# Performance work log

Hardware: AMD Instinct MI355X
Metric: run time of the kernel (lower is better)

The kernel has to match this reference:

```python
import jax, jax.numpy as jnp
import numpy as np

D = 128; DFF = 256; NH = 4; HD = D // NH
B = 8; T = 1024
PAIRS = [(0, 1), (1, 2), (0, 2)]  # (ABSTRACT,DYNAMIC),(DYNAMIC,CONCRETE),(ABSTRACT,CONCRETE)
BW = 0.5 / 3.0   # bridge_weight / len(BRIDGE_PAIRS)
LB_W = 0.01


def _hex_np():
    # itertools.product([-1,1], repeat=6): index i = 6-bit binary of i, MSB first, 0->-1
    bits = (np.arange(64)[:, None] >> np.arange(5, -1, -1)) & 1
    return (bits * 2.0 - 1.0).astype(np.float32)


def _anchors_np():
    h = _hex_np()
    idx = {'GEO': 0, 'HYDRO': 18, 'PYRO': 45, 'AERO': 6, 'COSMO': 27, 'NOOS': 63}
    a = (h[idx['NOOS']] + h[idx['COSMO']]) / 2.0   # ABSTRACT
    d = (h[idx['AERO']] + h[idx['PYRO']]) / 2.0    # DYNAMIC
    c = (h[idx['GEO']] + h[idx['HYDRO']]) / 2.0    # CONCRETE
    return np.stack([a, d, c]).astype(np.float32)


def _ln(x, g, b, eps=1e-5):
    m = x.mean(-1, keepdims=True)
    v = ((x - m) ** 2).mean(-1, keepdims=True)
    return (x - m) * jax.lax.rsqrt(v + eps) * g + b


def _mha(q, kv, in_w, out_w):
    # torch nn.MultiheadAttention, bias=False, batch_first
    Bq, Tq, _ = q.shape
    wq, wk, wv = in_w[:D], in_w[D:2 * D], in_w[2 * D:]
    Q = (q @ wq.T).reshape(Bq, Tq, NH, HD)
    K = (kv @ wk.T).reshape(Bq, Tq, NH, HD)
    V = (kv @ wv.T).reshape(Bq, Tq, NH, HD)
    scores = jnp.einsum('bqhd,bkhd->bhqk', Q, K) / jnp.sqrt(jnp.float32(HD))
    attn = jax.nn.softmax(scores, axis=-1)
    o = jnp.einsum('bhqk,bkhd->bqhd', attn, V).reshape(Bq, Tq, D)
    return o @ out_w.T


def setup_inputs() -> dict:
    key = jax.random.key(0)
    ks = iter(jax.random.split(key, 40))
    r = lambda shape, s=0.02: jax.random.normal(next(ks), shape, dtype=jnp.float32) * s
    return {
        'x': jax.random.normal(next(ks), (B, T, D), dtype=jnp.float32),
        'gr_norm_g': jnp.ones((D,), jnp.float32), 'gr_norm_b': jnp.zeros((D,), jnp.float32),
        'q6_w': r((6, D), 0.1),
        'log_temp': jnp.log(jnp.float32(0.5)),
        'grp_norm_g': jnp.ones((3, D), jnp.float32), 'grp_norm_b': jnp.zeros((3, D), jnp.float32),
        'grp_proj_w': r((3, 2, D), 0.1), 'grp_proj_b': jnp.zeros((3, 2), jnp.float32),
        'me_norm_g': jnp.ones((6, D), jnp.float32), 'me_norm_b': jnp.zeros((6, D), jnp.float32),
        'me_gate_w': r((6, DFF, D)), 'me_val_w': r((6, DFF, D)), 'me_out_w': r((6, D, DFF)),
        'br_in_w': r((3, 3 * D, D)), 'br_out_w': r((3, D, D)),
        'br_nq_g': jnp.ones((3, D), jnp.float32), 'br_nq_b': jnp.zeros((3, D), jnp.float32),
        'br_nkv_g': jnp.ones((3, D), jnp.float32), 'br_nkv_b': jnp.zeros((3, D), jnp.float32),
        'br_nffn_g': jnp.ones((3, D), jnp.float32), 'br_nffn_b': jnp.zeros((3, D), jnp.float32),
        'br_gate_w': r((3, 2 * D, D)), 'br_val_w': r((3, 2 * D, D)), 'br_ffn_out_w': r((3, D, 2 * D)),
        'br_gate': jnp.full((3,), -2.0, dtype=jnp.float32),
        'out_norm_g': jnp.ones((D,), jnp.float32), 'out_norm_b': jnp.zeros((D,), jnp.float32),
        'out_w': r((D, D)),
    }


def reference(x, gr_norm_g, gr_norm_b, q6_w, log_temp, grp_norm_g, grp_norm_b,
              grp_proj_w, grp_proj_b, me_norm_g, me_norm_b, me_gate_w, me_val_w,
              me_out_w, br_in_w, br_out_w, br_nq_g, br_nq_b, br_nkv_g, br_nkv_b,
              br_nffn_g, br_nffn_b, br_gate_w, br_val_w, br_ffn_out_w, br_gate,
              out_norm_g, out_norm_b, out_w):
    hexg = jnp.asarray(_hex_np())        # (64, 6)
    anchors = jnp.asarray(_anchors_np())  # (3, 6)

    # ---- GlobalRouter ----
    h = _ln(x, gr_norm_g, gr_norm_b)
    soft_bits = jnp.tanh(h @ q6_w.T)                       # (B,T,6)
    sim = soft_bits @ hexg.T                               # (B,T,64)
    temp = jnp.clip(jnp.exp(log_temp), 0.1, 5.0)
    hex_w = jax.nn.softmax(sim / temp, axis=-1)
    soft_hex = hex_w @ hexg                                # (B,T,6)
    group_weights = jax.nn.softmax(soft_hex @ anchors.T, axis=-1)  # (B,T,3)
    mw = group_weights.mean(axis=(0, 1))
    lb_total = -(mw * jnp.log(mw + 1e-8)).sum()

    # ---- all 6 micro experts (per-expert LayerNorm shares x's stats) ----
    m = x.mean(-1, keepdims=True)
    v = ((x - m) ** 2).mean(-1, keepdims=True)
    xn = (x - m) * jax.lax.rsqrt(v + 1e-5)                 # (B,T,D)
    hme = xn[None] * me_norm_g[:, None, None, :] + me_norm_b[:, None, None, :]  # (6,B,T,D)
    gate = jax.nn.silu(jnp.einsum('ebtd,efd->ebtf', hme, me_gate_w))
    val = jnp.einsum('ebtd,efd->ebtf', hme, me_val_w)
    eo = jnp.einsum('ebtf,edf->ebtd', gate * val, me_out_w)  # (6,B,T,D)

    # ---- per-group routing (2 experts each, top_k=2) ----
    group_outs = []
    for g in range(3):  # groups ordered [ABSTRACT, DYNAMIC, CONCRETE]; experts [2g, 2g+1]
        hg = xn * grp_norm_g[g] + grp_norm_b[g]
        logits = hg @ grp_proj_w[g].T + grp_proj_b[g]      # (B,T,2)
        w = jax.nn.softmax(logits, axis=-1)
        vals, idx = jax.lax.top_k(w, 2)                    # k = min(top_k=2, n=2)
        sparse = (jax.nn.one_hot(idx, 2, dtype=w.dtype) * vals[..., None]).sum(-2)
        sparse = sparse / (sparse.sum(-1, keepdims=True) + 1e-8)
        mwg = w.mean(axis=(0, 1))
        lb_total = lb_total - (mwg * jnp.log(mwg + 1e-8)).sum()
        go = sparse[..., 0:1] * eo[2 * g] + sparse[..., 1:2] * eo[2 * g + 1]
        group_outs.append(group_weights[..., g:g + 1] * go)

    # ---- bridge experts ----
    bridge_sum = jnp.zeros_like(x)
    for i, (a, b) in enumerate(PAIRS):
        xq, xk = group_outs[a], group_outs[b]
        qn = _ln(xq, br_nq_g[i], br_nq_b[i])
        kvn = _ln(xk, br_nkv_g[i], br_nkv_b[i])
        xb = xq + _mha(qn, kvn, br_in_w[i], br_out_w[i])
        hb = _ln(xb, br_nffn_g[i], br_nffn_b[i])
        ff = (jax.nn.silu(hb @ br_gate_w[i].T) * (hb @ br_val_w[i].T)) @ br_ffn_out_w[i].T
        xb = (xb + ff) * jax.nn.sigmoid(br_gate[i])
        bridge_sum = bridge_sum + BW * xb

    combined = group_outs[0] + group_outs[1] + group_outs[2] + bridge_sum
    out = _ln(combined, out_norm_g, out_norm_b) @ out_w.T
    return out, lb_total * LB_W
```

## Files before the change

kernel.cpp:

```cpp
#include <hip/hip_runtime.h>
#include <math.h>

#define DD    128
#define DFF   256
#define NHH   4
#define HDD   32
#define BB    8
#define TT    1024
#define NTOK  (BB*TT)
#define LDK   72
#define QKVN  384

#define WB_MEGATE 0
#define WB_MEVAL  196608
#define WB_MEOUT  393216
#define WB_BRIN   589824
#define WB_BROUT  737280
#define WB_BRG    786432
#define WB_BRV    884736
#define WB_BRF    983040
#define WB_OUTW   1081344
#define WB_TOT    1097728

typedef __bf16 bf16x8 __attribute__((ext_vector_type(8)));
typedef float  f32x4  __attribute__((ext_vector_type(4)));

__device__ __forceinline__ float wsum(float v){
#pragma unroll
  for(int o=32;o>0;o>>=1) v += __shfl_xor(v,o,64);
  return v;
}
__device__ __forceinline__ float wmaxr(float v){
#pragma unroll
  for(int o=32;o>0;o>>=1) v = fmaxf(v,__shfl_xor(v,o,64));
  return v;
}
__device__ __forceinline__ unsigned short f2bf(float x){
  __bf16 h = (__bf16)x;
  unsigned short u;
  __builtin_memcpy(&u, &h, 2);
  return u;
}

__device__ __forceinline__ void stage16(const float* __restrict__ gp,
                                        unsigned short* __restrict__ dst){
  float4 f0 = *reinterpret_cast<const float4*>(gp);
  float4 f1 = *reinterpret_cast<const float4*>(gp+4);
  float4 f2 = *reinterpret_cast<const float4*>(gp+8);
  float4 f3 = *reinterpret_cast<const float4*>(gp+12);
  float f[16] = {f0.x,f0.y,f0.z,f0.w, f1.x,f1.y,f1.z,f1.w,
                 f2.x,f2.y,f2.z,f2.w, f3.x,f3.y,f3.z,f3.w};
  unsigned short h[16];
#pragma unroll
  for(int j=0;j<16;j++) h[j] = f2bf(f[j]);
  *reinterpret_cast<uint4*>(dst)   = *reinterpret_cast<const uint4*>(h);
  *reinterpret_cast<uint4*>(dst+8) = *reinterpret_cast<const uint4*>(h+8);
}

__device__ __forceinline__ void stage16bf(const unsigned short* __restrict__ gp,
                                          unsigned short* __restrict__ dst){
  const uint4* s = reinterpret_cast<const uint4*>(gp);
  *reinterpret_cast<uint4*>(dst)   = s[0];
  *reinterpret_cast<uint4*>(dst+8) = s[1];
}

__device__ __forceinline__ void stageLN(const float* __restrict__ fr,
                                        float mean, float rstd,
                                        const float* __restrict__ g,
                                        const float* __restrict__ b,
                                        unsigned short* __restrict__ dst){
  unsigned short h[16];
#pragma unroll
  for(int j=0;j<16;j++){
    float y = (fr[j]-mean)*rstd*g[j] + b[j];
    h[j] = f2bf(y);
  }
  *reinterpret_cast<uint4*>(dst)   = *reinterpret_cast<const uint4*>(h);
  *reinterpret_cast<uint4*>(dst+8) = *reinterpret_cast<const uint4*>(h+8);
}

__global__ __launch_bounds__(256) void wconv(
    const float* __restrict__ a0, const float* __restrict__ a1, const float* __restrict__ a2,
    const float* __restrict__ a3, const float* __restrict__ a4, const float* __restrict__ a5,
    const float* __restrict__ a6, const float* __restrict__ a7, const float* __restrict__ a8,
    unsigned short* __restrict__ dst, float qsc){
  size_t i = ((size_t)blockIdx.x*256 + threadIdx.x)*4;
  if(i >= WB_TOT) return;
  const float* s; size_t off = i; float sc = 1.0f;
  if(i < WB_MEVAL){ s=a0; }
  else if(i < WB_MEOUT){ s=a1; off = i-WB_MEVAL; }
  else if(i < WB_BRIN ){ s=a2; off = i-WB_MEOUT; }
  else if(i < WB_BROUT){ s=a3; off = i-WB_BRIN;
    int row = (int)(off>>7); if((row % 384) < 128) sc = qsc; }
  else if(i < WB_BRG ){ s=a4; off = i-WB_BROUT; }
  else if(i < WB_BRV ){ s=a5; off = i-WB_BRG; }
  else if(i < WB_BRF ){ s=a6; off = i-WB_BRV; }
  else if(i < WB_OUTW){ s=a7; off = i-WB_BRF; }
  else { s=a8; off = i-WB_OUTW; }
  float4 v = *reinterpret_cast<const float4*>(s + off);
  unsigned short h4[4] = {f2bf(v.x*sc), f2bf(v.y*sc), f2bf(v.z*sc), f2bf(v.w*sc)};
  *reinterpret_cast<uint2*>(dst + i) = *reinterpret_cast<const uint2*>(h4);
}

__global__ __launch_bounds__(256) void routing_kernel(
    const float* __restrict__ x,
    const float* __restrict__ gr_g, const float* __restrict__ gr_b,
    const float* __restrict__ q6,   const float* __restrict__ logtemp,
    const float* __restrict__ grp_g,const float* __restrict__ grp_b,
    const float* __restrict__ gpw,  const float* __restrict__ gpb,
    float* __restrict__ gw_out, float* __restrict__ coef, float* __restrict__ part){
  __shared__ float sp[4][9];
  int lane = threadIdx.x & 63;
  int wv   = threadIdx.x >> 6;
  int t    = (blockIdx.x<<2) + wv;
  const float* xr = x + (size_t)t*DD;
  float r0 = xr[lane], r1 = xr[lane+64];
  float mn = wsum(r0+r1) * (1.0f/DD);
  float d0 = r0-mn, d1 = r1-mn;
  float vv = wsum(d0*d0 + d1*d1) * (1.0f/DD);
  float rstd = rsqrtf(vv + 1e-5f);
  float x0 = d0*rstd, x1 = d1*rstd;
  float h0 = x0*gr_g[lane]+gr_b[lane];
  float h1 = x1*gr_g[lane+64]+gr_b[lane+64];
  float sb[6];
#pragma unroll
  for(int j=0;j<6;j++){
    float p = h0*q6[j*DD+lane] + h1*q6[j*DD+lane+64];
    sb[j] = tanhf(wsum(p));
  }
  float sim = 0.f;
#pragma unroll
  for(int j=0;j<6;j++) sim += ((lane>>(5-j))&1) ? sb[j] : -sb[j];
  float temp = expf(logtemp[0]); temp = fminf(fmaxf(temp,0.1f),5.0f);
  float mx = wmaxr(sim);
  float p  = expf((sim-mx)/temp);
  float w  = p / wsum(p);
  float sh[6];
#pragma unroll
  for(int j=0;j<6;j++) sh[j] = wsum(((lane>>(5-j))&1) ? w : -w);
  const float A0[6]={0,1,1,0,1,1}, A1[6]={0,-1,0,1,0,0}, A2[6]={-1,0,-1,-1,0,-1};
  float l0=0,l1=0,l2=0;
#pragma unroll
  for(int j=0;j<6;j++){ l0+=sh[j]*A0[j]; l1+=sh[j]*A1[j]; l2+=sh[j]*A2[j]; }
  float m3 = fmaxf(l0,fmaxf(l1,l2));
  float e0=expf(l0-m3), e1=expf(l1-m3), e2=expf(l2-m3);
  float inv3 = 1.0f/(e0+e1+e2);
  float g0=e0*inv3, g1=e1*inv3, g2=e2*inv3;
  if(lane==0){ gw_out[t*3]=g0; gw_out[t*3+1]=g1; gw_out[t*3+2]=g2; }
  float gwv[3]={g0,g1,g2};
  float pw[6];
#pragma unroll
  for(int g=0; g<3; g++){
    float hg0 = x0*grp_g[g*DD+lane]    + grp_b[g*DD+lane];
    float hg1 = x1*grp_g[g*DD+lane+64] + grp_b[g*DD+lane+64];
    float q0 = wsum(hg0*gpw[(g*2+0)*DD+lane] + hg1*gpw[(g*2+0)*DD+lane+64]) + gpb[g*2+0];
    float q1 = wsum(hg0*gpw[(g*2+1)*DD+lane] + hg1*gpw[(g*2+1)*DD+lane+64]) + gpb[g*2+1];
    float mm = fmaxf(q0,q1);
    float a0 = expf(q0-mm), a1 = expf(q1-mm);
    float inv = 1.0f/(a0+a1);
    float w0 = a0*inv, w1 = a1*inv;
    pw[g*2]=w0; pw[g*2+1]=w1;
    float invs = 1.0f/(w0+w1+1e-8f);
    if(lane==0){
      coef[(size_t)(2*g  )*NTOK + t] = gwv[g]*w0*invs;
      coef[(size_t)(2*g+1)*NTOK + t] = gwv[g]*w1*invs;
    }
  }
  if(lane==0){
    sp[wv][0]=g0; sp[wv][1]=g1; sp[wv][2]=g2;
#pragma unroll
    for(int k=0;k<6;k++) sp[wv][3+k]=pw[k];
  }
  __syncthreads();
  if(threadIdx.x<9){
    part[blockIdx.x*9+threadIdx.x] =
      sp[0][threadIdx.x]+sp[1][threadIdx.x]+sp[2][threadIdx.x]+sp[3][threadIdx.x];
  }
}

__global__ __launch_bounds__(256) void lb_kernel(const float* __restrict__ part, float* __restrict__ outlb){
  __shared__ float sm[4][9];
  float acc[9] = {};
  for(int i=threadIdx.x; i<2048; i+=256){
#pragma unroll
    for(int c=0;c<9;c++) acc[c] += part[i*9+c];
  }
#pragma unroll
  for(int c=0;c<9;c++) acc[c] = wsum(acc[c]);
  int wv = threadIdx.x>>6, lane = threadIdx.x&63;
  if(lane==0){
#pragma unroll
    for(int c=0;c<9;c++) sm[wv][c]=acc[c];
  }
  __syncthreads();
  if(threadIdx.x==0){
    const float invN = 1.0f/(float)NTOK;
    float lb=0;
#pragma unroll
    for(int c=0;c<9;c++){
      float s = sm[0][c]+sm[1][c]+sm[2][c]+sm[3][c];
      float mw = s*invN;
      lb -= mw*logf(mw+1e-8f);
    }
    outlb[0] = lb*0.01f;
  }
}

template<int MODE,int LN,int ABF,int OBF,int PSEL,int RSEL,int SUM,int QKV>
__global__ __launch_bounds__(256) void gemm_mfma(
    const void* __restrict__ Ap, const unsigned short* __restrict__ W, void* __restrict__ Cp,
    int M, int N, int K,
    const float* __restrict__ sv, const float* __restrict__ bv,
    const float* __restrict__ resid, const float* __restrict__ gptr,
    size_t az, size_t wz, size_t cz, size_t pz, size_t rz, size_t gz){
  __shared__ unsigned short As[64*LDK];
  __shared__ unsigned short Ws[64*LDK];
  const int z = blockIdx.z;
  const float* A = (const float*)Ap;
  const unsigned short* Ab = (const unsigned short*)Ap;
  if(QKV){
    bool isQ = (blockIdx.x < 2);
    int s = isQ ? ((z==1)?1:0) : ((z==0)?1:2);
    A += (size_t)s*NTOK*DD;
    if(!isQ){ sv = resid; bv = gptr; }
  } else if(PSEL==0){ A += z*az; Ab += z*az; }
  else if(PSEL==1){ int s = (z==1)?1:0; A += (size_t)s*NTOK*DD; Ab += (size_t)s*NTOK*DD; }
  else            { int s = (z==0)?1:2; A += (size_t)s*NTOK*DD; Ab += (size_t)s*NTOK*DD; }
  W += z*wz;
  float* C = (float*)Cp + z*cz;
  unsigned short* Cb = (unsigned short*)Cp + z*cz;
  const float* rs = resid;
  if(RSEL==0) rs += z*rz;
  else { int s = (z==1)?1:0; rs += (size_t)s*NTOK*DD; }
  sv += z*pz; bv += z*pz;
  const float* gp2 = gptr + z*gz;
  int tid  = threadIdx.x;
  int m0   = blockIdx.y*64, n0 = blockIdx.x*64;
  int w    = tid>>6, lane = tid&63;
  int wr   = (w>>1)*32, wc = (w&1)*32;
  int r    = tid>>2, seg = (tid&3)*16;
  f32x4 acc[2][2] = {};
  auto step = [&](){
#pragma unroll
    for(int kk=0;kk<64;kk+=32){
      int ko = kk + (lane>>4)*8;
      bf16x8 a0 = *reinterpret_cast<const bf16x8*>(&As[(wr    + (lane&15))*LDK + ko]);
      bf16x8 a1 = *reinterpret_cast<const bf16x8*>(&As[(wr+16 + (lane&15))*LDK + ko]);
      bf16x8 b0 = *reinterpret_cast<const bf16x8*>(&Ws[(wc    + (lane&15))*LDK + ko]);
      bf16x8 b1 = *reinterpret_cast<const bf16x8*>(&Ws[(wc+16 + (lane&15))*LDK + ko]);
      acc[0][0] = __builtin_amdgcn_mfma_f32_16x16x32_bf16(a0,b0,acc[0][0],0,0,0);
      acc[0][1] = __builtin_amdgcn_mfma_f32_16x16x32_bf16(a0,b1,acc[0][1],0,0,0);
      acc[1][0] = __builtin_amdgcn_mfma_f32_16x16x32_bf16(a1,b0,acc[1][0],0,0,0);
      acc[1][1] = __builtin_amdgcn_mfma_f32_16x16x32_bf16(a1,b1,acc[1][1],0,0,0);
    }
  };
  if(LN){
    float fr[32]; float mean, rstd;
    if(SUM){
#pragma unroll
      for(int j=0;j<32;j++) fr[j]=0.f;
#pragma unroll
      for(int s=0;s<3;s++){
        const float* r1 = A     + (size_t)s*NTOK*DD + (size_t)(m0+r)*K + seg;
        const float* r2 = resid + (size_t)s*NTOK*DD + (size_t)(m0+r)*K + seg;
#pragma unroll
        for(int j=0;j<4;j++){
          float4 v1 = *reinterpret_cast<const float4*>(r1 + j*4);
          float4 v2 = *reinterpret_cast<const float4*>(r2 + j*4);
          fr[j*4]+=v1.x+v2.x; fr[j*4+1]+=v1.y+v2.y; fr[j*4+2]+=v1.z+v2.z; fr[j*4+3]+=v1.w+v2.w;
          float4 w1 = *reinterpret_cast<const float4*>(r1 + 64 + j*4);
          float4 w2 = *reinterpret_cast<const float4*>(r2 + 64 + j*4);
          fr[16+j*4]+=w1.x+w2.x; fr[16+j*4+1]+=w1.y+w2.y; fr[16+j*4+2]+=w1.z+w2.z; fr[16+j*4+3]+=w1.w+w2.w;
        }
      }
    } else {
      const float* arow = A + (size_t)(m0+r)*K + seg;
#pragma unroll
      for(int j=0;j<4;j++) *reinterpret_cast<float4*>(&fr[j*4])    = *reinterpret_cast<const float4*>(arow + j*4);
#pragma unroll
      for(int j=0;j<4;j++) *reinterpret_cast<float4*>(&fr[16+j*4]) = *reinterpret_cast<const float4*>(arow + 64 + j*4);
    }
    float s1=0.f, s2=0.f;
#pragma unroll
    for(int j=0;j<32;j++){ s1 += fr[j]; s2 += fr[j]*fr[j]; }
    s1 += __shfl_xor(s1,1,64); s1 += __shfl_xor(s1,2,64);
    s2 += __shfl_xor(s2,1,64); s2 += __shfl_xor(s2,2,64);
    mean = s1*(1.0f/DD);
    float var = s2*(1.0f/DD) - mean*mean;
    rstd = rsqrtf(var + 1e-5f);
#pragma unroll
    for(int kh=0; kh<2; ++kh){
      __syncthreads();
      stageLN(fr + kh*16, mean, rstd, sv + kh*64 + seg, bv + kh*64 + seg, &As[r*LDK + seg]);
      stage16bf(W + (size_t)(n0+r)*K + kh*64 + seg, &Ws[r*LDK + seg]);
      __syncthreads();
      step();
    }
  } else {
    for(int k0=0;k0<K;k0+=64){
      __syncthreads();
      if(ABF) stage16bf(Ab + (size_t)(m0+r)*K + k0 + seg, &As[r*LDK + seg]);
      else    stage16(A  + (size_t)(m0+r)*K + k0 + seg, &As[r*LDK + seg]);
      stage16bf(W + (size_t)(n0+r)*K + k0 + seg, &Ws[r*LDK + seg]);
      __syncthreads();
      step();
    }
  }
#pragma unroll
  for(int i=0;i<2;i++){
#pragma unroll
    for(int j=0;j<2;j++){
      int mb = m0 + wr + i*16 + (lane>>4)*4;
      int n  = n0 + wc + j*16 + (lane&15);
#pragma unroll
      for(int rg=0;rg<4;rg++){
        int m = mb + rg;
        float v = acc[i][j][rg];
        size_t o = (size_t)m*N + n;
        if(MODE==0){ if(OBF) Cb[o] = f2bf(v); else C[o] = v; }
        else if(MODE==3){ C[o] = rs[o] + v; }
        else if(MODE==5){
          float gs = (0.5f/3.0f)/(1.0f+expf(-gp2[0]));
          C[o] = gs*(rs[o]+v);
        }
      }
    }
  }
}

__global__ __launch_bounds__(256) void gemm_dual(
    const float* __restrict__ A, const unsigned short* __restrict__ G,
    const unsigned short* __restrict__ V,
    unsigned short* __restrict__ C, int M, int N, int K,
    const float* __restrict__ sv, const float* __restrict__ bv,
    size_t az, size_t wz, size_t cz, size_t pz){
  __shared__ unsigned short As[64*LDK];
  __shared__ unsigned short Gs[64*LDK];
  __shared__ unsigned short Vs[64*LDK];
  const int z = blockIdx.z;
  A += z*az; G += z*wz; V += z*wz; C += z*cz; sv += z*pz; bv += z*pz;
  int tid  = threadIdx.x;
  int m0   = blockIdx.y*64, n0 = blockIdx.x*64;
  int w    = tid>>6, lane = tid&63;
  int wr   = (w>>1)*32, wc = (w&1)*32;
  int r    = tid>>2, seg = (tid&3)*16;
  f32x4 accg[2][2] = {};
  f32x4 accv[2][2] = {};
  float fr[32]; float mean, rstd;
  {
    const float* arow = A + (size_t)(m0+r)*K + seg;
#pragma unroll
    for(int j=0;j<4;j++) *reinterpret_cast<float4*>(&fr[j*4])    = *reinterpret_cast<const float4*>(arow + j*4);
#pragma unroll
    for(int j=0;j<4;j++) *reinterpret_cast<float4*>(&fr[16+j*4]) = *reinterpret_cast<const float4*>(arow + 64 + j*4);
    float s1=0.f, s2=0.f;
#pragma unroll
    for(int j=0;j<32;j++){ s1 += fr[j]; s2 += fr[j]*fr[j]; }
    s1 += __shfl_xor(s1,1,64); s1 += __shfl_xor(s1,2,64);
    s2 += __shfl_xor(s2,1,64); s2 += __shfl_xor(s2,2,64);
    mean = s1*(1.0f/DD);
    float var = s2*(1.0f/DD) - mean*mean;
    rstd = rsqrtf(var + 1e-5f);
  }
#pragma unroll
  for(int kh=0; kh<2; ++kh){
    int k0 = kh*64;
    __syncthreads();
    stageLN(fr + kh*16, mean, rstd, sv + k0 + seg, bv + k0 + seg, &As[r*LDK + seg]);
    stage16bf(G + (size_t)(n0+r)*K + k0 + seg, &Gs[r*LDK + seg]);
    stage16bf(V + (size_t)(n0+r)*K + k0 + seg, &Vs[r*LDK + seg]);
    __syncthreads();
#pragma unroll
    for(int kk=0;kk<64;kk+=32){
      int ko = kk + (lane>>4)*8;
      bf16x8 a0 = *reinterpret_cast<const bf16x8*>(&As[(wr    + (lane&15))*LDK + ko]);
      bf16x8 a1 = *reinterpret_cast<const bf16x8*>(&As[(wr+16 + (lane&15))*LDK + ko]);
      bf16x8 g0 = *reinterpret_cast<const bf16x8*>(&Gs[(wc    + (lane&15))*LDK + ko]);
      bf16x8 g1 = *reinterpret_cast<const bf16x8*>(&Gs[(wc+16 + (lane&15))*LDK + ko]);
      bf16x8 v0 = *reinterpret_cast<const bf16x8*>(&Vs[(wc    + (lane&15))*LDK + ko]);
      bf16x8 v1 = *reinterpret_cast<const bf16x8*>(&Vs[(wc+16 + (lane&15))*LDK + ko]);
      accg[0][0] = __builtin_amdgcn_mfma_f32_16x16x32_bf16(a0,g0,accg[0][0],0,0,0);
      accg[0][1] = __builtin_amdgcn_mfma_f32_16x16x32_bf16(a0,g1,accg[0][1],0,0,0);
      accg[1][0] = __builtin_amdgcn_mfma_f32_16x16x32_bf16(a1,g0,accg[1][0],0,0,0);
      accg[1][1] = __builtin_amdgcn_mfma_f32_16x16x32_bf16(a1,g1,accg[1][1],0,0,0);
      accv[0][0] = __builtin_amdgcn_mfma_f32_16x16x32_bf16(a0,v0,accv[0][0],0,0,0);
      accv[0][1] = __builtin_amdgcn_mfma_f32_16x16x32_bf16(a0,v1,accv[0][1],0,0,0);
      accv[1][0] = __builtin_amdgcn_mfma_f32_16x16x32_bf16(a1,v0,accv[1][0],0,0,0);
      accv[1][1] = __builtin_amdgcn_mfma_f32_16x16x32_bf16(a1,v1,accv[1][1],0,0,0);
    }
  }
#pragma unroll
  for(int i=0;i<2;i++){
#pragma unroll
    for(int j=0;j<2;j++){
      int mb = m0 + wr + i*16 + (lane>>4)*4;
      int n  = n0 + wc + j*16 + (lane&15);
#pragma unroll
      for(int rg=0;rg<4;rg++){
        float gg = accg[i][j][rg];
        float vv = accv[i][j][rg];
        float sg = gg/(1.0f+expf(-gg));
        C[(size_t)(mb+rg)*N + n] = f2bf(sg*vv);
      }
    }
  }
}

__global__ __launch_bounds__(256) void gemm_moe2(
    const unsigned short* __restrict__ Ab, const unsigned short* __restrict__ Wb,
    float* __restrict__ Cb, const float* __restrict__ coef){
  __shared__ unsigned short As0[64*LDK];
  __shared__ unsigned short As1[64*LDK];
  __shared__ unsigned short Ws0[64*LDK];
  __shared__ unsigned short Ws1[64*LDK];
  const int g = blockIdx.z;
  const unsigned short* A0 = Ab + (size_t)(2*g)*NTOK*DFF;
  const unsigned short* A1 = A0 + (size_t)NTOK*DFF;
  const unsigned short* W0 = Wb + (size_t)(2*g)*DD*DFF;
  const unsigned short* W1 = W0 + (size_t)DD*DFF;
  float* C = Cb + (size_t)g*NTOK*DD;
  const float* c0 = coef + (size_t)(2*g)*NTOK;
  const float* c1 = c0 + NTOK;
  int tid  = threadIdx.x;
  int m0   = blockIdx.y*64, n0 = blockIdx.x*64;
  int w    = tid>>6, lane = tid&63;
  int wr   = (w>>1)*32, wc = (w&1)*32;
  int r    = tid>>2, seg = (tid&3)*16;
  f32x4 a0acc[2][2] = {};
  f32x4 a1acc[2][2] = {};
  for(int k0=0;k0<DFF;k0+=64){
    __syncthreads();
    stage16bf(A0 + (size_t)(m0+r)*DFF + k0 + seg, &As0[r*LDK + seg]);
    stage16bf(A1 + (size_t)(m0+r)*DFF + k0 + seg, &As1[r*LDK + seg]);
    stage16bf(W0 + (size_t)(n0+r)*DFF + k0 + seg, &Ws0[r*LDK + seg]);
    stage16bf(W1 + (size_t)(n0+r)*DFF + k0 + seg, &Ws1[r*LDK + seg]);
    __syncthreads();
#pragma unroll
    for(int kk=0;kk<64;kk+=32){
      int ko = kk + (lane>>4)*8;
      bf16x8 x00 = *reinterpret_cast<const bf16x8*>(&As0[(wr    + (lane&15))*LDK + ko]);
      bf16x8 x01 = *reinterpret_cast<const bf16x8*>(&As0[(wr+16 + (lane&15))*LDK + ko]);
      bf16x8 x10 = *reinterpret_cast<const bf16x8*>(&As1[(wr    + (lane&15))*LDK + ko]);
      bf16x8 x11 = *reinterpret_cast<const bf16x8*>(&As1[(wr+16 + (lane&15))*LDK + ko]);
      bf16x8 w00 = *reinterpret_cast<const bf16x8*>(&Ws0[(wc    + (lane&15))*LDK + ko]);
      bf16x8 w01 = *reinterpret_cast<const bf16x8*>(&Ws0[(wc+16 + (lane&15))*LDK + ko]);
      bf16x8 w10 = *reinterpret_cast<const bf16x8*>(&Ws1[(wc    + (lane&15))*LDK + ko]);
      bf16x8 w11 = *reinterpret_cast<const bf16x8*>(&Ws1[(wc+16 + (lane&15))*LDK + ko]);
      a0acc[0][0] = __builtin_amdgcn_mfma_f32_16x16x32_bf16(x00,w00,a0acc[0][0],0,0,0);
      a0acc[0][1] = __builtin_amdgcn_mfma_f32_16x16x32_bf16(x00,w01,a0acc[0][1],0,0,0);
      a0acc[1][0] = __builtin_amdgcn_mfma_f32_16x16x32_bf16(x01,w00,a0acc[1][0],0,0,0);
      a0acc[1][1] = __builtin_amdgcn_mfma_f32_16x16x32_bf16(x01,w01,a0acc[1][1],0,0,0);
      a1acc[0][0] = __builtin_amdgcn_mfma_f32_16x16x32_bf16(x10,w10,a1acc[0][0],0,0,0);
      a1acc[0][1] = __builtin_amdgcn_mfma_f32_16x16x32_bf16(x10,w11,a1acc[0][1],0,0,0);
      a1acc[1][0] = __builtin_amdgcn_mfma_f32_16x16x32_bf16(x11,w10,a1acc[1][0],0,0,0);
      a1acc[1][1] = __builtin_amdgcn_mfma_f32_16x16x32_bf16(x11,w11,a1acc[1][1],0,0,0);
    }
  }
#pragma unroll
  for(int i=0;i<2;i++){
#pragma unroll
    for(int j=0;j<2;j++){
      int mb = m0 + wr + i*16 + (lane>>4)*4;
      int n  = n0 + wc + j*16 + (lane&15);
#pragma unroll
      for(int rg=0;rg<4;rg++){
        int m = mb + rg;
        C[(size_t)m*DD + n] = c0[m]*a0acc[i][j][rg] + c1[m]*a1acc[i][j][rg];
      }
    }
  }
}

#define PSW(row) (((row)&8)<<1)
#define VSW(row) ((((row)>>3)&3)<<3)
__global__ __launch_bounds__(256) void attn_fused(
    const unsigned short* __restrict__ qkv,
    unsigned short* __restrict__ obuf){
  __shared__ __align__(16) unsigned short Ks[2][64*40];
  __shared__ __align__(16) unsigned short Vt[2][32*72];
  __shared__ __align__(16) unsigned short Vones[16*72];
  __shared__ __align__(16) unsigned short Ps[4][16*72];
  const int tid = threadIdx.x;
  const int w = tid>>6, lane = tid&63;
  const int lr = lane&15, lg = lane>>4;
  const int n_  = blockIdx.x;
  const int kx  = n_ & 7, jx = n_ >> 3;
  const int grp = kx*12 + (jx>>4);
  const int bx  = jx & 15;
  const int h   = grp & 3;
  const int b   = (grp>>2) & 7;
  const int br  = grp >> 5;
  const int qtok0 = b*TT + bx*64 + w*16;
  for(int idx=tid; idx<16*72; idx+=256)
    Vones[idx] = (idx < 64) ? (unsigned short)0x3F80 : (unsigned short)0;
  const unsigned short* qp = qkv + (size_t)br*NTOK*QKVN + (size_t)(qtok0 + lr)*QKVN + h*HDD + lg*8;
  bf16x8 qa = *reinterpret_cast<const bf16x8*>(qp);
  f32x4 o0 = {}, o1 = {}, o2 = {};
  float m[4] = {-1e30f,-1e30f,-1e30f,-1e30f};
  const unsigned short* KVbase = qkv + (size_t)br*NTOK*QKVN + (size_t)(b*TT)*QKVN + DD + h*HDD;
  const int skey0 = (tid    )>>3, sseg0 = ((tid    )&7)*4;
  const int skey1 = (tid+256)>>3, sseg1 = ((tid+256)&7)*4;

  {
    const unsigned short* s0 = KVbase + (size_t)skey0*QKVN + sseg0;
    const unsigned short* s1 = KVbase + (size_t)skey1*QKVN + sseg1;
    uint2 k0v = *reinterpret_cast<const uint2*>(s0);
    uint2 v0v = *reinterpret_cast<const uint2*>(s0 + DD);
    uint2 k1v = *reinterpret_cast<const uint2*>(s1);
    uint2 v1v = *reinterpret_cast<const uint2*>(s1 + DD);
    *reinterpret_cast<uint2*>(&Ks[0][skey0*40+sseg0]) = k0v;
    *reinterpret_cast<uint2*>(&Ks[0][skey1*40+sseg1]) = k1v;
    unsigned short vs[4];
    *reinterpret_cast<uint2*>(vs) = v0v;
    { const int kc = skey0 ^ VSW(sseg0);
      Vt[0][(sseg0  )*72+kc]=vs[0]; Vt[0][(sseg0+1)*72+kc]=vs[1];
      Vt[0][(sseg0+2)*72+kc]=vs[2]; Vt[0][(sseg0+3)*72+kc]=vs[3]; }
    *reinterpret_cast<uint2*>(vs) = v1v;
    { const int kc = skey1 ^ VSW(sseg1);
      Vt[0][(sseg1  )*72+kc]=vs[0]; Vt[0][(sseg1+1)*72+kc]=vs[1];
      Vt[0][(sseg1+2)*72+kc]=vs[2]; Vt[0][(sseg1+3)*72+kc]=vs[3]; }
  }
  __syncthreads();

  for(int t=0; t<16; t++){
    const int cur = t & 1;
    uint2 kn0, vn0, kn1, vn1;
    if(t < 15){
      const unsigned short* s0 = KVbase + (size_t)((t+1)*64 + skey0)*QKVN + sseg0;
      const unsigned short* s1 = KVbase + (size_t)((t+1)*64 + skey1)*QKVN + sseg1;
      kn0 = *reinterpret_cast<const uint2*>(s0);
      vn0 = *reinterpret_cast<const uint2*>(s0 + DD);
      kn1 = *reinterpret_cast<const uint2*>(s1);
      vn1 = *reinterpret_cast<const uint2*>(s1 + DD);
    }
    f32x4 s[4];
#pragma unroll
    for(int f=0;f<4;f++){
      bf16x8 kb = *reinterpret_cast<const bf16x8*>(&Ks[cur][(f*16+lr)*40 + lg*8]);
      f32x4 z = {};
      s[f] = __builtin_amdgcn_mfma_f32_16x16x32_bf16(qa,kb,z,0,0,0);
    }
    float tmax[4]; bool need=false;
#pragma unroll
    for(int r=0;r<4;r++){
      tmax[r] = fmaxf(fmaxf(s[0][r],s[1][r]),fmaxf(s[2][r],s[3][r]));
      need = need || (tmax[r] > m[r] + 8.0f);
    }
    if(__any(need)){
#pragma unroll
      for(int r=0;r<4;r++){
        float t2 = tmax[r];
#pragma unroll
        for(int off=1;off<16;off<<=1) t2 = fmaxf(t2,__shfl_xor(t2,off,64));
        float nm = fmaxf(m[r],t2);
        float sc = __builtin_amdgcn_exp2f(m[r]-nm);
        m[r] = nm; o0[r] *= sc; o1[r] *= sc; o2[r] *= sc;
      }
    }
#pragma unroll
    for(int r=0;r<4;r++){
      const int q = lg*4+r;
      const int cw = PSW(q);
#pragma unroll
      for(int f=0;f<4;f++){
        float p = __builtin_amdgcn_exp2f(s[f][r]-m[r]);
        Ps[w][q*72 + ((f*16+lr)^cw)] = f2bf(p);
      }
    }
    const int pw_ = PSW(lr);
    bf16x8 pa0 = *reinterpret_cast<const bf16x8*>(&Ps[w][lr*72 + ((lg*8   )^pw_)]);
    bf16x8 pa1 = *reinterpret_cast<const bf16x8*>(&Ps[w][lr*72 + ((lg*8+32)^pw_)]);
    {
      const int r_ = lr, vw = VSW(r_);
      bf16x8 vb0 = *reinterpret_cast<const bf16x8*>(&Vt[cur][r_*72 + ((lg*8   )^vw)]);
      bf16x8 vb1 = *reinterpret_cast<const bf16x8*>(&Vt[cur][r_*72 + ((lg*8+32)^vw)]);
      o0 = __builtin_amdgcn_mfma_f32_16x16x32_bf16(pa0,vb0,o0,0,0,0);
      o0 = __builtin_amdgcn_mfma_f32_16x16x32_bf16(pa1,vb1,o0,0,0,0);
    }
    {
      const int r_ = 16+lr, vw = VSW(r_);
      bf16x8 vb0 = *reinterpret_cast<const bf16x8*>(&Vt[cur][(r_-16)*72 + ((lg*8   )^vw)+16*72]);
      bf16x8 vb1 = *reinterpret_cast<const bf16x8*>(&Vt[cur][(r_-16)*72 + ((lg*8+32)^vw)+16*72]);
      o1 = __builtin_amdgcn_mfma_f32_16x16x32_bf16(pa0,vb0,o1,0,0,0);
      o1 = __builtin_amdgcn_mfma_f32_16x16x32_bf16(pa1,vb1,o1,0,0,0);
    }
    {
      const int r_ = 32+lr, vw = VSW(r_);
      bf16x8 vb0 = *reinterpret_cast<const bf16x8*>(&Vones[lr*72 + ((lg*8   )^vw)]);
      bf16x8 vb1 = *reinterpret_cast<const bf16x8*>(&Vones[lr*72 + ((lg*8+32)^vw)]);
      o2 = __builtin_amdgcn_mfma_f32_16x16x32_bf16(pa0,vb0,o2,0,0,0);
      o2 = __builtin_amdgcn_mfma_f32_16x16x32_bf16(pa1,vb1,o2,0,0,0);
    }
    if(t < 15){
      const int nb = cur ^ 1;
      *reinterpret_cast<uint2*>(&Ks[nb][skey0*40+sseg0]) = kn0;
      *reinterpret_cast<uint2*>(&Ks[nb][skey1*40+sseg1]) = kn1;
      unsigned short vs[4];
      *reinterpret_cast<uint2*>(vs) = vn0;
      { const int kc = skey0 ^ VSW(sseg0);
        Vt[nb][(sseg0  )*72+kc]=vs[0]; Vt[nb][(sseg0+1)*72+kc]=vs[1];
        Vt[nb][(sseg0+2)*72+kc]=vs[2]; Vt[nb][(sseg0+3)*72+kc]=vs[3]; }
      *reinterpret_cast<uint2*>(vs) = vn1;
      { const int kc = skey1 ^ VSW(sseg1);
        Vt[nb][(sseg1  )*72+kc]=vs[0]; Vt[nb][(sseg1+1)*72+kc]=vs[1];
        Vt[nb][(sseg1+2)*72+kc]=vs[2]; Vt[nb][(sseg1+3)*72+kc]=vs[3]; }
    }
    __syncthreads();
  }
#pragma unroll
  for(int r=0;r<4;r++){
    float lsr = __shfl(o2[r], lane & 48, 64);
    float inv = 1.0f/lsr;
    int row = qtok0 + lg*4 + r;
    unsigned short* orow = obuf + (size_t)br*NTOK*DD + (size_t)row*DD + h*HDD;
    orow[lr]    = f2bf(o0[r]*inv);
    orow[16+lr] = f2bf(o1[r]*inv);
  }
}

extern "C" void kernel_launch(void* const* d_in, const int* in_sizes, int n_in,
                              void* d_out, int out_size, void* d_ws, size_t ws_size,
                              hipStream_t stream){
  (void)in_sizes; (void)n_in; (void)out_size; (void)ws_size;
  const float* x       = (const float*)d_in[0];
  const float* gr_g    = (const float*)d_in[1];
  const float* gr_b    = (const float*)d_in[2];
  const float* q6_w    = (const float*)d_in[3];
  const float* logtemp = (const float*)d_in[4];
  const float* grp_g   = (const float*)d_in[5];
  const float* grp_b   = (const float*)d_in[6];
  const float* gpw     = (const float*)d_in[7];
  const float* gpb     = (const float*)d_in[8];
  const float* me_g    = (const float*)d_in[9];
  const float* me_b    = (const float*)d_in[10];
  const float* me_gate = (const float*)d_in[11];
  const float* me_val  = (const float*)d_in[12];
  const float* me_out  = (const float*)d_in[13];
  const float* br_in   = (const float*)d_in[14];
  const float* br_outw = (const float*)d_in[15];
  const float* nq_g    = (const float*)d_in[16];
  const float* nq_b    = (const float*)d_in[17];
  const float* nkv_g   = (const float*)d_in[18];
  const float* nkv_b   = (const float*)d_in[19];
  const float* nff_g   = (const float*)d_in[20];
  const float* nff_b   = (const float*)d_in[21];
  const float* brg_w   = (const float*)d_in[22];
  const float* brv_w   = (const float*)d_in[23];
  const float* brf_w   = (const float*)d_in[24];
  const float* br_gate = (const float*)d_in[25];
  const float* on_g    = (const float*)d_in[26];
  const float* on_b    = (const float*)d_in[27];
  const float* out_w   = (const float*)d_in[28];
  float* out = (float*)d_out;
  float* ws  = (float*)d_ws;

  float* coef  = ws;
  float* part  = ws + 65536;
  unsigned short* gvb6 = (unsigned short*)(ws + 131072);
  float* go    = ws + 6731072;
  unsigned short* qkv  = (unsigned short*)(ws + 9900000);
  unsigned short* obuf = (unsigned short*)(ws + 14700000);
  unsigned short* wbf  = (unsigned short*)(ws + 21400000);
  float* xb    = ws + 23000000;
  unsigned short* gvb2 = (unsigned short*)(ws + 26200000);
  float* bsum  = ws + 29400000;
  float* gw    = ws + 32700000;

  const float qscale = 0.17677669529663687f * 1.4426950408889634f;

  wconv<<<1072,256,0,stream>>>(me_gate, me_val, me_out, br_in, br_outw,
                               brg_w, brv_w, brf_w, out_w, wbf, qscale);

  routing_kernel<<<2048,256,0,stream>>>(x, gr_g, gr_b, q6_w, logtemp,
                                        grp_g, grp_b, gpw, gpb, gw, coef, part);
  lb_kernel<<<1,256,0,stream>>>(part, out + 1048576);

  gemm_dual<<<dim3(4,128,6),256,0,stream>>>(x, wbf+WB_MEGATE, wbf+WB_MEVAL, gvb6,
      NTOK,DFF,DD, me_g, me_b, 0, (size_t)DFF*DD, (size_t)NTOK*DFF, DD);
  gemm_moe2<<<dim3(2,128,3),256,0,stream>>>(gvb6, wbf+WB_MEOUT, go, coef);

  gemm_mfma<0,1,0,1,0,0,0,1><<<dim3(6,128,3),256,0,stream>>>(go, wbf+WB_BRIN, qkv,
      NTOK,QKVN,DD, nq_g, nq_b, nkv_g, nkv_b,
      0, (size_t)QKVN*DD, (size_t)NTOK*QKVN, DD, 0, 0);
  attn_fused<<<1536,256,0,stream>>>(qkv, obuf);
  gemm_mfma<3,0,1,0,0,1,0,0><<<dim3(2,128,3),256,0,stream>>>(obuf, wbf+WB_BROUT, xb,
      NTOK,DD,DD, nullptr, nullptr, go, nullptr,
      (size_t)NTOK*DD, (size_t)DD*DD, (size_t)NTOK*DD, 0, 0, 0);
  gemm_dual<<<dim3(4,128,3),256,0,stream>>>(xb, wbf+WB_BRG, wbf+WB_BRV, gvb2,
      NTOK,2*DD,DD, nff_g, nff_b, (size_t)NTOK*DD, (size_t)2*DD*DD, (size_t)NTOK*2*DD, DD);
  gemm_mfma<5,0,1,0,0,0,0,0><<<dim3(2,128,3),256,0,stream>>>(gvb2, wbf+WB_BRF, bsum,
      NTOK,DD,2*DD, nullptr, nullptr, xb, br_gate,
      (size_t)NTOK*2*DD, (size_t)DD*2*DD, (size_t)NTOK*DD, 0, (size_t)NTOK*DD, 1);

  gemm_mfma<0,1,0,0,0,0,1,0><<<dim3(2,128,1),256,0,stream>>>(go, wbf+WB_OUTW, out,
      NTOK,DD,DD, on_g, on_b, bsum, nullptr,
      0, 0, 0, 0, 0, 0);
}
```

Before: 191.1 us.

## Process 128 queries per attention block with 8 waves sharing K/V tiles

The attention kernel now runs 512 threads (8 waves) per block, each block covering 128 query rows instead of 64, and the grid is halved. Each K/V tile staged in shared memory is reused by twice as many query waves, which halves global K/V traffic and staging work per query. Each thread now loads one K/V segment instead of two. The cost is fewer blocks, larger per-block shared memory for P buffers, and wider barriers that may lower occupancy or add sync stalls.

```diff
diff --git a/kernel.cpp b/kernel.cpp
--- a/kernel.cpp
+++ b/kernel.cpp
@@ -473,65 +473,53 @@
 
 #define PSW(row) (((row)&8)<<1)
 #define VSW(row) ((((row)>>3)&3)<<3)
-__global__ __launch_bounds__(256) void attn_fused(
+__global__ __launch_bounds__(512) void attn_fused(
     const unsigned short* __restrict__ qkv,
     unsigned short* __restrict__ obuf){
   __shared__ __align__(16) unsigned short Ks[2][64*40];
   __shared__ __align__(16) unsigned short Vt[2][32*72];
   __shared__ __align__(16) unsigned short Vones[16*72];
-  __shared__ __align__(16) unsigned short Ps[4][16*72];
+  __shared__ __align__(16) unsigned short Ps[8][16*72];
   const int tid = threadIdx.x;
   const int w = tid>>6, lane = tid&63;
   const int lr = lane&15, lg = lane>>4;
   const int n_  = blockIdx.x;
   const int kx  = n_ & 7, jx = n_ >> 3;
-  const int grp = kx*12 + (jx>>4);
-  const int bx  = jx & 15;
+  const int grp = kx*12 + (jx>>3);
+  const int bx  = jx & 7;
   const int h   = grp & 3;
   const int b   = (grp>>2) & 7;
   const int br  = grp >> 5;
-  const int qtok0 = b*TT + bx*64 + w*16;
-  for(int idx=tid; idx<16*72; idx+=256)
+  const int qtok0 = b*TT + bx*128 + w*16;
+  for(int idx=tid; idx<16*72; idx+=512)
     Vones[idx] = (idx < 64) ? (unsigned short)0x3F80 : (unsigned short)0;
   const unsigned short* qp = qkv + (size_t)br*NTOK*QKVN + (size_t)(qtok0 + lr)*QKVN + h*HDD + lg*8;
   bf16x8 qa = *reinterpret_cast<const bf16x8*>(qp);
   f32x4 o0 = {}, o1 = {}, o2 = {};
   float m[4] = {-1e30f,-1e30f,-1e30f,-1e30f};
   const unsigned short* KVbase = qkv + (size_t)br*NTOK*QKVN + (size_t)(b*TT)*QKVN + DD + h*HDD;
-  const int skey0 = (tid    )>>3, sseg0 = ((tid    )&7)*4;
-  const int skey1 = (tid+256)>>3, sseg1 = ((tid+256)&7)*4;
+  const int skey = tid>>3, sseg = (tid&7)*4;
 
   {
-    const unsigned short* s0 = KVbase + (size_t)skey0*QKVN + sseg0;
-    const unsigned short* s1 = KVbase + (size_t)skey1*QKVN + sseg1;
-    uint2 k0v = *reinterpret_cast<const uint2*>(s0);
-    uint2 v0v = *reinterpret_cast<const uint2*>(s0 + DD);
-    uint2 k1v = *reinterpret_cast<const uint2*>(s1);
-    uint2 v1v = *reinterpret_cast<const uint2*>(s1 + DD);
-    *reinterpret_cast<uint2*>(&Ks[0][skey0*40+sseg0]) = k0v;
-    *reinterpret_cast<uint2*>(&Ks[0][skey1*40+sseg1]) = k1v;
+    const unsigned short* s0 = KVbase + (size_t)skey*QKVN + sseg;
+    uint2 kv = *reinterpret_cast<const uint2*>(s0);
+    uint2 vv = *reinterpret_cast<const uint2*>(s0 + DD);
+    *reinterpret_cast<uint2*>(&Ks[0][skey*40+sseg]) = kv;
     unsigned short vs[4];
-    *reinterpret_cast<uint2*>(vs) = v0v;
-    { const int kc = skey0 ^ VSW(sseg0);
-      Vt[0][(sseg0  )*72+kc]=vs[0]; Vt[0][(sseg0+1)*72+kc]=vs[1];
-      Vt[0][(sseg0+2)*72+kc]=vs[2]; Vt[0][(sseg0+3)*72+kc]=vs[3]; }
-    *reinterpret_cast<uint2*>(vs) = v1v;
-    { const int kc = skey1 ^ VSW(sseg1);
-      Vt[0][(sseg1  )*72+kc]=vs[0]; Vt[0][(sseg1+1)*72+kc]=vs[1];
-      Vt[0][(sseg1+2)*72+kc]=vs[2]; Vt[0][(sseg1+3)*72+kc]=vs[3]; }
+    *reinterpret_cast<uint2*>(vs) = vv;
+    const int kc = skey ^ VSW(sseg);
+    Vt[0][(sseg  )*72+kc]=vs[0]; Vt[0][(sseg+1)*72+kc]=vs[1];
+    Vt[0][(sseg+2)*72+kc]=vs[2]; Vt[0][(sseg+3)*72+kc]=vs[3];
   }
   __syncthreads();
 
   for(int t=0; t<16; t++){
     const int cur = t & 1;
-    uint2 kn0, vn0, kn1, vn1;
+    uint2 kn, vn;
     if(t < 15){
-      const unsigned short* s0 = KVbase + (size_t)((t+1)*64 + skey0)*QKVN + sseg0;
-      const unsigned short* s1 = KVbase + (size_t)((t+1)*64 + skey1)*QKVN + sseg1;
-      kn0 = *reinterpret_cast<const uint2*>(s0);
-      vn0 = *reinterpret_cast<const uint2*>(s0 + DD);
-      kn1 = *reinterpret_cast<const uint2*>(s1);
-      vn1 = *reinterpret_cast<const uint2*>(s1 + DD);
+      const unsigned short* s0 = KVbase + (size_t)((t+1)*64 + skey)*QKVN + sseg;
+      kn = *reinterpret_cast<const uint2*>(s0);
+      vn = *reinterpret_cast<const uint2*>(s0 + DD);
     }
     f32x4 s[4];
 #pragma unroll
@@ -593,17 +581,12 @@
     }
     if(t < 15){
       const int nb = cur ^ 1;
-      *reinterpret_cast<uint2*>(&Ks[nb][skey0*40+sseg0]) = kn0;
-      *reinterpret_cast<uint2*>(&Ks[nb][skey1*40+sseg1]) = kn1;
+      *reinterpret_cast<uint2*>(&Ks[nb][skey*40+sseg]) = kn;
       unsigned short vs[4];
-      *reinterpret_cast<uint2*>(vs) = vn0;
-      { const int kc = skey0 ^ VSW(sseg0);
-        Vt[nb][(sseg0  )*72+kc]=vs[0]; Vt[nb][(sseg0+1)*72+kc]=vs[1];
-        Vt[nb][(sseg0+2)*72+kc]=vs[2]; Vt[nb][(sseg0+3)*72+kc]=vs[3]; }
-      *reinterpret_cast<uint2*>(vs) = vn1;
-      { const int kc = skey1 ^ VSW(sseg1);
-        Vt[nb][(sseg1  )*72+kc]=vs[0]; Vt[nb][(sseg1+1)*72+kc]=vs[1];
-        Vt[nb][(sseg1+2)*72+kc]=vs[2]; Vt[nb][(sseg1+3)*72+kc]=vs[3]; }
+      *reinterpret_cast<uint2*>(vs) = vn;
+      const int kc = skey ^ VSW(sseg);
+      Vt[nb][(sseg  )*72+kc]=vs[0]; Vt[nb][(sseg+1)*72+kc]=vs[1];
+      Vt[nb][(sseg+2)*72+kc]=vs[2]; Vt[nb][(sseg+3)*72+kc]=vs[3];
     }
     __syncthreads();
   }
@@ -682,7 +665,7 @@
   gemm_mfma<0,1,0,1,0,0,0,1><<<dim3(6,128,3),256,0,stream>>>(go, wbf+WB_BRIN, qkv,
       NTOK,QKVN,DD, nq_g, nq_b, nkv_g, nkv_b,
       0, (size_t)QKVN*DD, (size_t)NTOK*QKVN, DD, 0, 0);
-  attn_fused<<<1536,256,0,stream>>>(qkv, obuf);
+  attn_fused<<<768,512,0,stream>>>(qkv, obuf);
   gemm_mfma<3,0,1,0,0,1,0,0><<<dim3(2,128,3),256,0,stream>>>(obuf, wbf+WB_BROUT, xb,
       NTOK,DD,DD, nullptr, nullptr, go, nullptr,
       (size_t)NTOK*DD, (size_t)DD*DD, (size_t)NTOK*DD, 0, 0, 0);
```

Result: faster. 184.1 us (-3.6%).
